# Kernel tuning notes

Hardware: AMD Instinct MI355X
Metric: run time of the kernel (lower is better)

The kernel has to match this reference:

```python
import jax, jax.numpy as jnp
import numpy as np

B, D, DEPTH, H, E, N, NC = 128, 192, 12, 3, 4, 65, 100
WIN_HALF = 3  # window_size=7 -> |i-j| <= 3


def _ln(x, g, b, eps=1e-5):
    m = x.mean(-1, keepdims=True)
    v = ((x - m) ** 2).mean(-1, keepdims=True)
    return (x - m) / jnp.sqrt(v + eps) * g + b


def _forward(x, conv_w, conv_b, pe_g, pe_b, cls_token, pos_embed,
             n1_g, n1_b, qkv_w, temp, proj_w, proj_b, n2_g, n2_b,
             gate_w, gate_b, e_w1, e_b1, e_w2, e_b2, attn_scale, mlp_scale,
             norm_g, norm_b, hc_w, hc_b, head_w, head_b):
    Bx = x.shape[0]
    # patch embed: conv with kernel==stride==4 is a blocked matmul
    p = x.reshape(Bx, 3, 8, 4, 8, 4).transpose(0, 2, 4, 1, 3, 5).reshape(Bx, 64, 48)
    t = p @ conv_w.reshape(D, 48).T + conv_b
    t = _ln(t, pe_g, pe_b)
    t = jnp.concatenate([jnp.broadcast_to(cls_token, (Bx, 1, D)), t], axis=1) + pos_embed
    Nn = t.shape[1]
    hd = D // H
    scale = hd ** -0.5
    idx = jnp.arange(Nn)
    # local-window attention mask (log of {0,1} -> {-inf,0})
    mask = jnp.where(jnp.abs(idx[:, None] - idx[None, :]) <= WIN_HALF, 0.0, -jnp.inf)
    for l in range(DEPTH):
        # --- attention ---
        y = _ln(t, n1_g[l], n1_b[l])
        qkv = (y @ qkv_w[l].T).reshape(Bx, Nn, 3, H, hd).transpose(2, 0, 3, 1, 4)
        q, k, v = qkv[0], qkv[1], qkv[2]
        a = (q @ k.transpose(0, 1, 3, 2)) * scale / temp[l]  # [B,H,N,N]
        a = jax.nn.softmax(a + mask, axis=-1)
        o = (a @ v).transpose(0, 2, 1, 3).reshape(Bx, Nn, D)
        o = o @ proj_w[l].T + proj_b[l]
        t = t + attn_scale[l] * o
        # --- top-2 MoE (dense-equivalent of the masked per-expert dispatch) ---
        y = _ln(t, n2_g[l], n2_b[l])
        g = jax.nn.softmax(y @ gate_w[l].T + gate_b[l], axis=-1)  # [B,N,E]
        tg, ti = jax.lax.top_k(g, 2)
        tg = tg / tg.sum(-1, keepdims=True)
        h = jax.nn.gelu(jnp.einsum('bnc,ehc->bneh', y, e_w1[l]) + e_b1[l], approximate=False)
        eo = jnp.einsum('bneh,ech->bnec', h, e_w2[l]) + e_b2[l]  # [B,N,E,C]
        sel = jnp.take_along_axis(eo, ti[..., None], axis=2)  # [B,N,2,C]
        mo = (sel * tg[..., None]).sum(axis=2)
        t = t + mlp_scale[l] * mo
    t = _ln(t, norm_g, norm_b)
    cls = t[:, 0]
    # hypercomplex linear head: out[:,k] += x[:,j] @ W[(k-j)%n].T
    xv = cls.reshape(Bx, E, D // E)
    perm = (jnp.arange(E)[:, None] - jnp.arange(E)[None, :]) % E  # [k,j] -> i
    hh = jnp.einsum('bjc,kjoc->bko', xv, hc_w[perm]).reshape(Bx, 2 * D) + hc_b
    hh = jax.nn.gelu(hh, approximate=False)
    return hh @ head_w.T + head_b


def setup_inputs() -> dict:
    ks = iter(jax.random.split(jax.random.key(0), 64))
    def rn(shape, s=0.02):
        return jax.random.normal(next(ks), shape, jnp.float32) * s
    return dict(
        x=jax.random.normal(next(ks), (B, 3, 32, 32), jnp.float32),
        conv_w=rn((D, 3, 4, 4)), conv_b=jnp.zeros((D,)),
        pe_g=jnp.ones((D,)), pe_b=jnp.zeros((D,)),
        cls_token=rn((1, 1, D)), pos_embed=rn((1, N, D)),
        n1_g=jnp.ones((DEPTH, D)), n1_b=jnp.zeros((DEPTH, D)),
        qkv_w=rn((DEPTH, 3 * D, D)), temp=jnp.ones((DEPTH, H, 1, 1)),
        proj_w=rn((DEPTH, D, D)), proj_b=jnp.zeros((DEPTH, D)),
        n2_g=jnp.ones((DEPTH, D)), n2_b=jnp.zeros((DEPTH, D)),
        gate_w=rn((DEPTH, E, D)), gate_b=jnp.zeros((DEPTH, E)),
        e_w1=rn((DEPTH, E, 2 * D, D)), e_b1=jnp.zeros((DEPTH, E, 2 * D)),
        e_w2=rn((DEPTH, E, D, 2 * D)), e_b2=jnp.zeros((DEPTH, E, D)),
        attn_scale=jnp.ones((DEPTH,)), mlp_scale=jnp.ones((DEPTH,)),
        norm_g=jnp.ones((D,)), norm_b=jnp.zeros((D,)),
        hc_w=rn((E, 2 * D // E, D // E)), hc_b=jnp.zeros((2 * D,)),
        head_w=rn((NC, 2 * D)), head_b=jnp.zeros((NC,)),
    )


def reference(x, conv_w, conv_b, pe_g, pe_b, cls_token, pos_embed,
              n1_g, n1_b, qkv_w, temp, proj_w, proj_b, n2_g, n2_b,
              gate_w, gate_b, e_w1, e_b1, e_w2, e_b2, attn_scale, mlp_scale,
              norm_g, norm_b, hc_w, hc_b, head_w, head_b):
    return _forward(x, conv_w, conv_b, pe_g, pe_b, cls_token, pos_embed,
                    n1_g, n1_b, qkv_w, temp, proj_w, proj_b, n2_g, n2_b,
                    gate_w, gate_b, e_w1, e_b1, e_w2, e_b2, attn_scale, mlp_scale,
                    norm_g, norm_b, hc_w, hc_b, head_w, head_b)
```

## Files before the change

### kernel.cpp

```cpp
#include <hip/hip_runtime.h>
#include <cmath>

#define ROWS 8320
#define DD   192

typedef __attribute__((ext_vector_type(8))) _Float16 half8;
typedef __attribute__((ext_vector_type(4))) float floatx4;

#define GLD16(gp, lp) __builtin_amdgcn_global_load_lds( \
    (const __attribute__((address_space(1))) void*)(gp), \
    (__attribute__((address_space(3))) void*)(lp), 16, 0, 0)

#define MFMA_F16 __builtin_amdgcn_mfma_f32_16x16x32_f16

__device__ __forceinline__ float gelu_f(float x) {
    return 0.5f * x * (1.0f + erff(x * 0.70710678118654752440f));
}

__device__ __forceinline__ float blk_sum_192(float v, float* sbuf) {
    int tid = threadIdx.x;
    sbuf[tid] = v;
    __syncthreads();
    for (int off = 96; off >= 3; off >>= 1) {
        if (tid < off) sbuf[tid] += sbuf[tid + off];
        __syncthreads();
    }
    float r = sbuf[0] + sbuf[1] + sbuf[2];
    __syncthreads();
    return r;
}

__global__ __launch_bounds__(256) void cvt_h_kernel(
    const float* __restrict__ s, _Float16* __restrict__ d, long n8)
{
    long i = (long)blockIdx.x * 256 + threadIdx.x;
    if (i >= n8) return;
    const float* sp = s + i * 8;
    _Float16* dp = d + i * 8;
    #pragma unroll
    for (int j = 0; j < 8; j++) dp[j] = (_Float16)sp[j];
}

__global__ __launch_bounds__(256) void permw2h_kernel(
    const float* __restrict__ s, _Float16* __restrict__ d)
{
    long i = (long)blockIdx.x * 256 + threadIdx.x;
    if (i >= (long)12 * 192 * 192) return;
    int l = (int)(i / (192 * 192));
    int rem = (int)(i % (192 * 192));
    int n = rem / 192, p = rem % 192;
    int c0 = p * 8;
    int e = c0 / 384, k0 = c0 % 384;
    const float* sp = s + (((size_t)l * 4 + e) * 192 + n) * 384 + k0;
    _Float16* dp = d + i * 8;
    #pragma unroll
    for (int j = 0; j < 8; j++) dp[j] = (_Float16)sp[j];
}

__global__ __launch_bounds__(192) void embed_kernel(
    const float* __restrict__ x, const float* __restrict__ conv_w,
    const float* __restrict__ conv_b, const float* __restrict__ pe_g,
    const float* __restrict__ pe_b, const float* __restrict__ cls_tok,
    const float* __restrict__ pos, float* __restrict__ t)
{
    __shared__ float patch[48];
    __shared__ float red[192];
    int blk = blockIdx.x;
    int b = blk / 65, n = blk % 65;
    int tid = threadIdx.x;
    if (n == 0) {
        t[(size_t)b * 65 * DD + tid] = cls_tok[tid] + pos[tid];
        return;
    }
    int p = n - 1, gy = p / 8, gx = p % 8;
    if (tid < 48) {
        int c = tid / 16, iy = (tid % 16) / 4, ix = tid % 4;
        patch[tid] = x[((size_t)b * 3 + c) * 1024 + (size_t)(gy * 4 + iy) * 32 + (gx * 4 + ix)];
    }
    __syncthreads();
    float s = conv_b[tid];
    const float* w = conv_w + (size_t)tid * 48;
    #pragma unroll
    for (int f = 0; f < 48; f++) s += patch[f] * w[f];
    float mean = blk_sum_192(s, red) * (1.0f / 192.0f);
    float d = s - mean;
    float var = blk_sum_192(d * d, red) * (1.0f / 192.0f);
    float o = d * rsqrtf(var + 1e-5f) * pe_g[tid] + pe_b[tid];
    t[((size_t)b * 65 + n) * DD + tid] = o + pos[(size_t)n * DD + tid];
}

__global__ __launch_bounds__(256) void ln_kernel(
    const float* __restrict__ in, const float* __restrict__ ctb,
    float* __restrict__ tout,
    float* __restrict__ yf, _Float16* __restrict__ yh,
    const float* __restrict__ g, const float* __restrict__ bb, long in_stride, int nrows,
    const float* __restrict__ gwm, const float* __restrict__ gb,
    int4* __restrict__ gwout)
{
    int wave = threadIdx.x >> 6, lane = threadIdx.x & 63;
    int r = blockIdx.x * 4 + wave;
    if (r >= nrows) return;
    const float* row = in + (size_t)r * in_stride;
    float v0 = row[lane], v1 = row[lane + 64], v2 = row[lane + 128];
    if (ctb) {
        long gr = (long)r * (in_stride / DD);
        const float* cb = ctb + gr * 384;
        v0 += cb[lane] + cb[192 + lane];
        v1 += cb[lane + 64] + cb[256 + lane];
        v2 += cb[lane + 128] + cb[320 + lane];
        if (tout) {
            float* tr = tout + (size_t)r * in_stride;
            tr[lane] = v0; tr[lane + 64] = v1; tr[lane + 128] = v2;
        }
    }
    float s = v0 + v1 + v2;
    #pragma unroll
    for (int off = 32; off > 0; off >>= 1) s += __shfl_xor(s, off);
    float mean = s * (1.0f / 192.0f);
    float d0 = v0 - mean, d1 = v1 - mean, d2 = v2 - mean;
    float q = d0 * d0 + d1 * d1 + d2 * d2;
    #pragma unroll
    for (int off = 32; off > 0; off >>= 1) q += __shfl_xor(q, off);
    float rstd = rsqrtf(q * (1.0f / 192.0f) + 1e-5f);
    float o0 = d0 * rstd * g[lane] + bb[lane];
    float o1 = d1 * rstd * g[lane + 64] + bb[lane + 64];
    float o2 = d2 * rstd * g[lane + 128] + bb[lane + 128];
    if (yf) {
        float* yr = yf + (size_t)r * DD;
        yr[lane] = o0; yr[lane + 64] = o1; yr[lane + 128] = o2;
    }
    if (yh) {
        _Float16* yr = yh + (size_t)r * DD;
        yr[lane] = (_Float16)o0; yr[lane + 64] = (_Float16)o1; yr[lane + 128] = (_Float16)o2;
    }
    if (gwm) {
        float pe[4];
        #pragma unroll
        for (int e = 0; e < 4; e++) {
            const float* w = gwm + (size_t)e * DD;
            pe[e] = o0 * w[lane] + o1 * w[lane + 64] + o2 * w[lane + 128];
            #pragma unroll
            for (int off = 32; off > 0; off >>= 1) pe[e] += __shfl_xor(pe[e], off);
        }
        if (lane == 0) {
            #pragma unroll
            for (int e = 0; e < 4; e++) pe[e] += gb[e];
            float mx = fmaxf(fmaxf(pe[0], pe[1]), fmaxf(pe[2], pe[3]));
            float ex[4];
            #pragma unroll
            for (int e = 0; e < 4; e++) ex[e] = expf(pe[e] - mx);
            int i0 = 0;
            #pragma unroll
            for (int e = 1; e < 4; e++) if (ex[e] > ex[i0]) i0 = e;
            int i1 = (i0 == 0) ? 1 : 0;
            #pragma unroll
            for (int e = 0; e < 4; e++) if (e != i0 && ex[e] > ex[i1]) i1 = e;
            float denom = ex[i0] + ex[i1];
            int4 o4;
            o4.x = i0; o4.y = i1;
            o4.z = __float_as_int(ex[i0] / denom);
            o4.w = __float_as_int(ex[i1] / denom);
            gwout[r] = o4;
        }
    }
}

__global__ __launch_bounds__(256) void gate_build_kernel(
    const int4* __restrict__ gwrow, int* __restrict__ cnt,
    int* __restrict__ list, float* __restrict__ wlist, int rows)
{
    int r = blockIdx.x * 256 + threadIdx.x;
    int lane = threadIdx.x & 63;
    bool active = r < rows;
    int4 gv = active ? gwrow[r] : int4{-1, -1, 0, 0};
    #pragma unroll
    for (int e = 0; e < 4; e++) {
        bool sel = active && (gv.x == e || gv.y == e);
        int rank = (gv.x == e) ? 0 : 1;
        float w = (gv.x == e) ? __int_as_float(gv.z) : __int_as_float(gv.w);
        unsigned long long mask = __ballot(sel);
        int cw = __popcll(mask);
        if (cw) {
            int leader = __ffsll((long long)mask) - 1;
            int base = 0;
            if (lane == leader) base = atomicAdd(&cnt[e], cw);
            base = __shfl(base, leader);
            if (sel) {
                int idx = base + __popcll(mask & ((1ULL << lane) - 1ULL));
                list[(size_t)e * ROWS + idx] = (r << 1) | rank;
                wlist[(size_t)e * ROWS + idx] = w;
            }
        }
    }
}

template <int MODE>
__global__ __launch_bounds__(256) void gemm_h(
    const _Float16* __restrict__ A, const _Float16* __restrict__ W,
    int Nn, _Float16* __restrict__ outH, float* __restrict__ t,
    const float* __restrict__ bias, const float* __restrict__ scale)
{
    __shared__ __align__(16) _Float16 As[64 * 192];
    __shared__ __align__(16) _Float16 Ws[64 * 192];
    const int tid = threadIdx.x;
    const int lane = tid & 63, wave = tid >> 6;
    const int m0 = blockIdx.x * 64, n0 = blockIdx.y * 64;
    const int wm = (wave & 1) * 32, wn = (wave >> 1) * 32;
    const int lr = lane & 15, quad = lane >> 4;

    #pragma unroll
    for (int i = 0; i < 6; i++) {
        int s = (wave * 6 + i) * 64 + lane;
        int rr = s / 24, c = s % 24;
        GLD16(A + (size_t)(m0 + rr) * 192 + (c ^ (rr & 7)) * 8,
              (char*)As + (size_t)(wave * 6 + i) * 1024);
        GLD16(W + (size_t)(n0 + rr) * 192 + (c ^ (rr & 7)) * 8,
              (char*)Ws + (size_t)(wave * 6 + i) * 1024);
    }
    __syncthreads();

    floatx4 zero = {0.f, 0.f, 0.f, 0.f};
    floatx4 acc[2][2];
    acc[0][0] = zero; acc[0][1] = zero; acc[1][0] = zero; acc[1][1] = zero;

    #pragma unroll
    for (int m = 0; m < 6; m++) {
        int ch = m * 4 + quad;
        half8 a[2], w[2];
        #pragma unroll
        for (int ti = 0; ti < 2; ti++) {
            int ar = wm + ti * 16 + lr;
            a[ti] = *(const half8*)(As + ((size_t)ar * 24 + (ch ^ (ar & 7))) * 8);
            int cr = wn + ti * 16 + lr;
            w[ti] = *(const half8*)(Ws + ((size_t)cr * 24 + (ch ^ (cr & 7))) * 8);
        }
        #pragma unroll
        for (int ti = 0; ti < 2; ti++)
            #pragma unroll
            for (int tj = 0; tj < 2; tj++)
                acc[ti][tj] = MFMA_F16(a[ti], w[tj], acc[ti][tj], 0, 0, 0);
    }

    float sc = (MODE == 2) ? scale[0] : 0.f;
    #pragma unroll
    for (int ti = 0; ti < 2; ti++)
        #pragma unroll
        for (int tj = 0; tj < 2; tj++)
            #pragma unroll
            for (int r = 0; r < 4; r++) {
                int grow = m0 + wm + ti * 16 + quad * 4 + r;
                int gcol = n0 + wn + tj * 16 + lr;
                float v = acc[ti][tj][r];
                if (MODE == 0) {
                    float vp = __shfl_xor(v, 1);
                    if ((lane & 1) == 0) {
                        union { _Float16 h[2]; unsigned u; } pk;
                        pk.h[0] = (_Float16)v;
                        pk.h[1] = (_Float16)vp;
                        *(unsigned*)(outH + (size_t)grow * Nn + (gcol & ~1)) = pk.u;
                    }
                } else {
                    t[(size_t)grow * DD + gcol] += sc * (v + bias[gcol]);
                }
            }
}

__global__ __launch_bounds__(256) void moe_kernel(
    const _Float16* __restrict__ yh, const _Float16* __restrict__ w1,
    const _Float16* __restrict__ w2, const float* __restrict__ b1,
    const float* __restrict__ b2, const float* __restrict__ scale,
    const int* __restrict__ cnt, const int* __restrict__ list,
    const float* __restrict__ wlist, float* __restrict__ ctb)
{
    __shared__ __align__(16) _Float16 As[32 * 192];
    __shared__ __align__(16) _Float16 W1s[64 * 192];
    __shared__ __align__(16) _Float16 W2s[192 * 64];
    __shared__ __align__(16) _Float16 Hs[32 * 64];
    __shared__ int   rl[32];
    __shared__ int   rk[32];
    __shared__ float wl[32];
    const int e  = blockIdx.y;
    const int cnte = cnt[e];
    const int r0 = blockIdx.x * 32;
    if (r0 >= cnte) return;
    const int tid = threadIdx.x;
    const int lane = tid & 63, wave = tid >> 6;
    const int lr = lane & 15, quad = lane >> 4;
    const int wr = (wave & 1) * 16;
    const int wc1 = (wave >> 1) * 16;
    const int wc2 = (wave >> 1) * 96;

    if (tid < 32) {
        int sl = r0 + tid;
        bool ok = sl < cnte;
        int v = ok ? list[(size_t)e * ROWS + sl] : 0;
        rl[tid] = ok ? (v >> 1) : 0;
        rk[tid] = ok ? (v & 1) : -1;
        wl[tid] = ok ? wlist[(size_t)e * ROWS + sl] : 0.f;
    }
    __syncthreads();

    #pragma unroll
    for (int i = 0; i < 3; i++) {
        int s = (wave * 3 + i) * 64 + lane;
        int rr = s / 24, c = s % 24;
        GLD16(yh + (size_t)rl[rr] * 192 + (c ^ (rr & 7)) * 8,
              (char*)As + (size_t)(wave * 3 + i) * 1024);
    }
    #pragma unroll
    for (int i = 0; i < 6; i++) {
        int s = (wave * 6 + i) * 64 + lane;
        int rr = s / 24, c = s % 24;
        GLD16(w1 + ((size_t)e * 384 + rr) * 192 + (c ^ (rr & 7)) * 8,
              (char*)W1s + (size_t)(wave * 6 + i) * 1024);
    }
    __syncthreads();

    floatx4 zero = {0.f, 0.f, 0.f, 0.f};
    floatx4 acc2[6];
    #pragma unroll
    for (int j = 0; j < 6; j++) acc2[j] = zero;

    for (int nc = 0; nc < 6; nc++) {
        int ncg = e * 6 + nc;
        #pragma unroll
        for (int i = 0; i < 6; i++) {
            int s = (wave * 6 + i) * 64 + lane;
            int n = s >> 3, c = s & 7;
            GLD16(w2 + (size_t)n * 1536 + (ncg * 8 + (c ^ (n & 7))) * 8,
                  (char*)W2s + (size_t)(wave * 6 + i) * 1024);
        }
        floatx4 acc1[2];
        acc1[0] = zero; acc1[1] = zero;
        #pragma unroll
        for (int m = 0; m < 6; m++) {
            int ar = wr + lr;
            int ch = m * 4 + quad;
            half8 a = *(const half8*)(As + ((size_t)ar * 24 + (ch ^ (ar & 7))) * 8);
            #pragma unroll
            for (int tc = 0; tc < 2; tc++) {
                int cr = wc1 + tc * 32 + lr;
                half8 w = *(const half8*)(W1s + ((size_t)cr * 24 + (ch ^ (cr & 7))) * 8);
                acc1[tc] = MFMA_F16(a, w, acc1[tc], 0, 0, 0);
            }
        }
        #pragma unroll
        for (int tc = 0; tc < 2; tc++)
            #pragma unroll
            for (int r = 0; r < 4; r++) {
                int hrow = wr + quad * 4 + r;
                int hcol = wc1 + tc * 32 + lr;
                float v = gelu_f(acc1[tc][r] + b1[64 * ncg + hcol]) * wl[hrow];
                float vp = __shfl_xor(v, 1);
                if ((lane & 1) == 0) {
                    union { _Float16 h[2]; unsigned u; } pk;
                    pk.h[0] = (_Float16)v;
                    pk.h[1] = (_Float16)vp;
                    int cl = (hcol >> 3) ^ (hrow & 7);
                    *(unsigned*)(Hs + ((size_t)hrow * 8 + cl) * 8 + (hcol & 7)) = pk.u;
                }
            }
        __syncthreads();
        if (nc < 5) {
            #pragma unroll
            for (int i = 0; i < 6; i++) {
                int s = (wave * 6 + i) * 64 + lane;
                int rr = s / 24, c = s % 24;
                GLD16(w1 + ((size_t)e * 384 + (nc + 1) * 64 + rr) * 192 + (c ^ (rr & 7)) * 8,
                      (char*)W1s + (size_t)(wave * 6 + i) * 1024);
            }
        }
        #pragma unroll
        for (int kk = 0; kk < 2; kk++) {
            int ar = wr + lr;
            int ch = kk * 4 + quad;
            half8 a = *(const half8*)(Hs + ((size_t)ar * 8 + (ch ^ (ar & 7))) * 8);
            #pragma unroll
            for (int tj = 0; tj < 6; tj++) {
                int cr = wc2 + tj * 16 + lr;
                half8 w = *(const half8*)(W2s + ((size_t)cr * 8 + (ch ^ (cr & 7))) * 8);
                acc2[tj] = MFMA_F16(a, w, acc2[tj], 0, 0, 0);
            }
        }
        __syncthreads();
    }

    float sc = scale[0];
    #pragma unroll
    for (int tj = 0; tj < 6; tj++) {
        int gcol = wc2 + tj * 16 + lr;
        #pragma unroll
        for (int r = 0; r < 4; r++) {
            int lrow = wr + quad * 4 + r;
            int rank = rk[lrow];
            if (rank >= 0) {
                float v = sc * (acc2[tj][r] + wl[lrow] * b2[e * 192 + gcol]);
                ctb[((size_t)rl[lrow] * 2 + rank) * 192 + gcol] = v;
            }
        }
    }
}

__global__ __launch_bounds__(256) void attn_kernel(
    const _Float16* __restrict__ qkv, const float* __restrict__ temp,
    _Float16* __restrict__ o)
{
    __shared__ float q[65][64], k[65][64], v[65][64];
    __shared__ float p[65][8];
    int bh = blockIdx.x;
    int b = bh / 3, h = bh % 3;
    int tid = threadIdx.x;
    float coef = 0.125f / temp[h];
    const _Float16* base = qkv + (size_t)b * 65 * 576 + h * 64;
    for (int idx = tid; idx < 65 * 64; idx += 256) {
        int i = idx >> 6, d = idx & 63;
        q[i][d] = (float)base[(size_t)i * 576 + d];
        k[i][d] = (float)base[(size_t)i * 576 + 192 + d];
        v[i][d] = (float)base[(size_t)i * 576 + 384 + d];
    }
    __syncthreads();
    if (tid < 65) {
        int i = tid;
        float sc[7];
        float mx = -1e30f;
        #pragma unroll
        for (int jo = 0; jo < 7; jo++) {
            int j = i - 3 + jo;
            if (j >= 0 && j < 65) {
                float s = 0.f;
                #pragma unroll
                for (int d = 0; d < 64; d++) s += q[i][d] * k[j][d];
                sc[jo] = s * coef;
                mx = fmaxf(mx, sc[jo]);
            } else sc[jo] = -1e30f;
        }
        float sum = 0.f;
        #pragma unroll
        for (int jo = 0; jo < 7; jo++) {
            float e = expf(sc[jo] - mx);
            p[i][jo] = e;
            sum += e;
        }
        float inv = 1.0f / sum;
        #pragma unroll
        for (int jo = 0; jo < 7; jo++) p[i][jo] *= inv;
    }
    __syncthreads();
    for (int idx = tid; idx < 65 * 64; idx += 256) {
        int i = idx >> 6, d = idx & 63;
        float s = 0.f;
        #pragma unroll
        for (int jo = 0; jo < 7; jo++) {
            int j = i - 3 + jo;
            if (j >= 0 && j < 65) s += p[i][jo] * v[j][d];
        }
        o[((size_t)b * 65 + i) * 192 + h * 64 + d] = (_Float16)s;
    }
}

__global__ __launch_bounds__(128) void head_kernel(
    const float* __restrict__ cls, const float* __restrict__ hc_w,
    const float* __restrict__ hc_b, const float* __restrict__ head_w,
    const float* __restrict__ head_b, float* __restrict__ out)
{
    __shared__ float c[192];
    __shared__ float hh[384];
    int b = blockIdx.x, tid = threadIdx.x;
    for (int i = tid; i < 192; i += 128) c[i] = cls[(size_t)b * 192 + i];
    __syncthreads();
    for (int i = tid; i < 384; i += 128) {
        int k = i / 96, o = i % 96;
        float s = hc_b[i];
        #pragma unroll
        for (int j = 0; j < 4; j++) {
            int pp = (k - j + 4) & 3;
            const float* w = hc_w + ((size_t)pp * 96 + o) * 48;
            const float* xv = c + j * 48;
            #pragma unroll
            for (int cc = 0; cc < 48; cc++) s += xv[cc] * w[cc];
        }
        hh[i] = gelu_f(s);
    }
    __syncthreads();
    for (int i = tid; i < 100; i += 128) {
        float s = head_b[i];
        const float* w = head_w + (size_t)i * 384;
        for (int kk = 0; kk < 384; kk++) s += hh[kk] * w[kk];
        out[(size_t)b * 100 + i] = s;
    }
}

extern "C" void kernel_launch(void* const* d_in, const int* in_sizes, int n_in,
                              void* d_out, int out_size, void* d_ws, size_t ws_size,
                              hipStream_t stream)
{
    const float* x        = (const float*)d_in[0];
    const float* conv_w   = (const float*)d_in[1];
    const float* conv_b   = (const float*)d_in[2];
    const float* pe_g     = (const float*)d_in[3];
    const float* pe_b     = (const float*)d_in[4];
    const float* cls_tok  = (const float*)d_in[5];
    const float* pos      = (const float*)d_in[6];
    const float* n1_g     = (const float*)d_in[7];
    const float* n1_b     = (const float*)d_in[8];
    const float* qkv_w    = (const float*)d_in[9];
    const float* temp     = (const float*)d_in[10];
    const float* proj_w   = (const float*)d_in[11];
    const float* proj_b   = (const float*)d_in[12];
    const float* n2_g     = (const float*)d_in[13];
    const float* n2_b     = (const float*)d_in[14];
    const float* gate_w   = (const float*)d_in[15];
    const float* gate_b   = (const float*)d_in[16];
    const float* e_w1     = (const float*)d_in[17];
    const float* e_b1     = (const float*)d_in[18];
    const float* e_w2     = (const float*)d_in[19];
    const float* e_b2     = (const float*)d_in[20];
    const float* attn_sc  = (const float*)d_in[21];
    const float* mlp_sc   = (const float*)d_in[22];
    const float* norm_g   = (const float*)d_in[23];
    const float* norm_b   = (const float*)d_in[24];
    const float* hc_w     = (const float*)d_in[25];
    const float* hc_b     = (const float*)d_in[26];
    const float* head_w   = (const float*)d_in[27];
    const float* head_b   = (const float*)d_in[28];

    char* base = (char*)d_ws;
    float*  t     = (float*)base;   base += (size_t)ROWS * DD * 4;
    float*  ctb   = (float*)base;   base += (size_t)ROWS * 384 * 4;
    int4*   gwrow = (int4*)base;    base += (size_t)ROWS * 16;
    int*    cnts  = (int*)base;     base += (size_t)12 * 4 * sizeof(int) + 64;
    int*    elist = (int*)base;     base += (size_t)4 * ROWS * 4;
    float*  ewls  = (float*)base;   base += (size_t)4 * ROWS * 4;
    float*  ycls  = (float*)base;   base += (size_t)128 * DD * 4;
    _Float16* yhb = (_Float16*)base; base += (size_t)ROWS * DD * 2;
    _Float16* qkvh = (_Float16*)base; base += (size_t)ROWS * 576 * 2;
    _Float16* osph = (_Float16*)base; base += (size_t)ROWS * DD * 2;
    _Float16* qkvw_h = (_Float16*)base; base += (size_t)12 * 576 * 192 * 2;
    _Float16* projw_h = (_Float16*)base; base += (size_t)12 * 192 * 192 * 2;
    _Float16* ew1_h = (_Float16*)base; base += (size_t)12 * 1536 * 192 * 2;
    _Float16* ew2_h = (_Float16*)base; base += (size_t)12 * 192 * 1536 * 2;

    hipMemsetAsync(cnts, 0, 12 * 4 * sizeof(int), stream);

    {
        long n8 = (long)12 * 576 * 192 / 8;
        cvt_h_kernel<<<(int)((n8 + 255) / 256), 256, 0, stream>>>(qkv_w, qkvw_h, n8);
        n8 = (long)12 * 192 * 192 / 8;
        cvt_h_kernel<<<(int)((n8 + 255) / 256), 256, 0, stream>>>(proj_w, projw_h, n8);
        n8 = (long)12 * 1536 * 192 / 8;
        cvt_h_kernel<<<(int)((n8 + 255) / 256), 256, 0, stream>>>(e_w1, ew1_h, n8);
        long n = (long)12 * 192 * 192;
        permw2h_kernel<<<(int)((n + 255) / 256), 256, 0, stream>>>(e_w2, ew2_h);
    }

    embed_kernel<<<128 * 65, 192, 0, stream>>>(x, conv_w, conv_b, pe_g, pe_b, cls_tok, pos, t);

    for (int l = 0; l < 12; l++) {
        ln_kernel<<<ROWS / 4, 256, 0, stream>>>(
            t, (l > 0) ? ctb : nullptr, (l > 0) ? t : nullptr,
            nullptr, yhb, n1_g + l * DD, n1_b + l * DD, DD, ROWS,
            nullptr, nullptr, nullptr);
        gemm_h<0><<<dim3(130, 9), 256, 0, stream>>>(
            yhb, qkvw_h + (size_t)l * 576 * 192, 576, qkvh, nullptr, nullptr, nullptr);
        attn_kernel<<<128 * 3, 256, 0, stream>>>(qkvh, temp + l * 3, osph);
        gemm_h<2><<<dim3(130, 3), 256, 0, stream>>>(
            osph, projw_h + (size_t)l * 192 * 192, 192, nullptr, t,
            proj_b + l * DD, attn_sc + l);
        ln_kernel<<<ROWS / 4, 256, 0, stream>>>(
            t, nullptr, nullptr, nullptr, yhb, n2_g + l * DD, n2_b + l * DD, DD, ROWS,
            gate_w + (size_t)l * 4 * DD, gate_b + l * 4, gwrow);
        gate_build_kernel<<<(ROWS + 255) / 256, 256, 0, stream>>>(
            gwrow, cnts + l * 4, elist, ewls, ROWS);
        moe_kernel<<<dim3(260, 4), 256, 0, stream>>>(
            yhb, ew1_h + (size_t)l * 1536 * 192, ew2_h + (size_t)l * 192 * 1536,
            e_b1 + (size_t)l * 1536, e_b2 + (size_t)l * 4 * 192, mlp_sc + l,
            cnts + l * 4, elist, ewls, ctb);
    }

    ln_kernel<<<32, 256, 0, stream>>>(
        t, ctb, nullptr, ycls, nullptr, norm_g, norm_b, (long)65 * DD, 128,
        nullptr, nullptr, nullptr);
    head_kernel<<<128, 128, 0, stream>>>(ycls, hc_w, hc_b, head_w, head_b, (float*)d_out);
}
```

Before: 1.352 ms.

## Scatter MoE output via atomics into residual and load A rows into registers

The MoE kernel now adds its expert outputs straight into the residual stream t with float atomicAdd. This replaces writing per-rank rows to a separate ctb buffer that the next layernorm had to read back and sum. It also loads each wave's gathered A rows straight from global memory into registers, dropping the LDS staging of activations and the shared row/weight tables. The attention kernel's shared arrays are padded to 65 columns to reduce bank conflicts. The cost is atomic contention on t, with two experts per row, and a summation order that is no longer deterministic.

Result: faster. 1.152 ms (-14.8%).

```diff
diff --git a/kernel.cpp b/kernel.cpp
--- a/kernel.cpp
+++ b/kernel.cpp
@@ -176,7 +176,6 @@
     #pragma unroll
     for (int e = 0; e < 4; e++) {
         bool sel = active && (gv.x == e || gv.y == e);
-        int rank = (gv.x == e) ? 0 : 1;
         float w = (gv.x == e) ? __int_as_float(gv.z) : __int_as_float(gv.w);
         unsigned long long mask = __ballot(sel);
         int cw = __popcll(mask);
@@ -187,6 +186,7 @@
             base = __shfl(base, leader);
             if (sel) {
                 int idx = base + __popcll(mask & ((1ULL << lane) - 1ULL));
+                int rank = (gv.x == e) ? 0 : 1;
                 list[(size_t)e * ROWS + idx] = (r << 1) | rank;
                 wlist[(size_t)e * ROWS + idx] = w;
             }
@@ -270,15 +270,11 @@
     const _Float16* __restrict__ w2, const float* __restrict__ b1,
     const float* __restrict__ b2, const float* __restrict__ scale,
     const int* __restrict__ cnt, const int* __restrict__ list,
-    const float* __restrict__ wlist, float* __restrict__ ctb)
-{
-    __shared__ __align__(16) _Float16 As[32 * 192];
+    const float* __restrict__ wlist, float* __restrict__ t)
+{
     __shared__ __align__(16) _Float16 W1s[64 * 192];
     __shared__ __align__(16) _Float16 W2s[192 * 64];
     __shared__ __align__(16) _Float16 Hs[32 * 64];
-    __shared__ int   rl[32];
-    __shared__ int   rk[32];
-    __shared__ float wl[32];
     const int e  = blockIdx.y;
     const int cnte = cnt[e];
     const int r0 = blockIdx.x * 32;
@@ -290,23 +286,6 @@
     const int wc1 = (wave >> 1) * 16;
     const int wc2 = (wave >> 1) * 96;
 
-    if (tid < 32) {
-        int sl = r0 + tid;
-        bool ok = sl < cnte;
-        int v = ok ? list[(size_t)e * ROWS + sl] : 0;
-        rl[tid] = ok ? (v >> 1) : 0;
-        rk[tid] = ok ? (v & 1) : -1;
-        wl[tid] = ok ? wlist[(size_t)e * ROWS + sl] : 0.f;
-    }
-    __syncthreads();
-
-    #pragma unroll
-    for (int i = 0; i < 3; i++) {
-        int s = (wave * 3 + i) * 64 + lane;
-        int rr = s / 24, c = s % 24;
-        GLD16(yh + (size_t)rl[rr] * 192 + (c ^ (rr & 7)) * 8,
-              (char*)As + (size_t)(wave * 3 + i) * 1024);
-    }
     #pragma unroll
     for (int i = 0; i < 6; i++) {
         int s = (wave * 6 + i) * 64 + lane;
@@ -314,6 +293,29 @@
         GLD16(w1 + ((size_t)e * 384 + rr) * 192 + (c ^ (rr & 7)) * 8,
               (char*)W1s + (size_t)(wave * 6 + i) * 1024);
     }
+
+    int sl = r0 + wr + lr;
+    int rv = -1; float wv = 0.f;
+    if (sl < cnte) {
+        rv = list[(size_t)e * ROWS + sl];
+        wv = wlist[(size_t)e * ROWS + sl];
+    }
+    int arow = (rv >= 0) ? (rv >> 1) : 0;
+
+    half8 a[6];
+    {
+        const _Float16* ap = yh + (size_t)arow * 192 + quad * 8;
+        #pragma unroll
+        for (int m = 0; m < 6; m++) a[m] = *(const half8*)(ap + m * 32);
+    }
+
+    int rvr[4]; float bwr[4];
+    #pragma unroll
+    for (int r = 0; r < 4; r++) {
+        rvr[r] = __shfl(rv, quad * 4 + r);
+        bwr[r] = __shfl(wv, quad * 4 + r);
+    }
+
     __syncthreads();
 
     floatx4 zero = {0.f, 0.f, 0.f, 0.f};
@@ -334,14 +336,12 @@
         acc1[0] = zero; acc1[1] = zero;
         #pragma unroll
         for (int m = 0; m < 6; m++) {
-            int ar = wr + lr;
             int ch = m * 4 + quad;
-            half8 a = *(const half8*)(As + ((size_t)ar * 24 + (ch ^ (ar & 7))) * 8);
             #pragma unroll
             for (int tc = 0; tc < 2; tc++) {
                 int cr = wc1 + tc * 32 + lr;
                 half8 w = *(const half8*)(W1s + ((size_t)cr * 24 + (ch ^ (cr & 7))) * 8);
-                acc1[tc] = MFMA_F16(a, w, acc1[tc], 0, 0, 0);
+                acc1[tc] = MFMA_F16(a[m], w, acc1[tc], 0, 0, 0);
             }
         }
         #pragma unroll
@@ -350,7 +350,7 @@
             for (int r = 0; r < 4; r++) {
                 int hrow = wr + quad * 4 + r;
                 int hcol = wc1 + tc * 32 + lr;
-                float v = gelu_f(acc1[tc][r] + b1[64 * ncg + hcol]) * wl[hrow];
+                float v = gelu_f(acc1[tc][r] + b1[64 * ncg + hcol]) * bwr[r];
                 float vp = __shfl_xor(v, 1);
                 if ((lane & 1) == 0) {
                     union { _Float16 h[2]; unsigned u; } pk;
@@ -374,12 +374,12 @@
         for (int kk = 0; kk < 2; kk++) {
             int ar = wr + lr;
             int ch = kk * 4 + quad;
-            half8 a = *(const half8*)(Hs + ((size_t)ar * 8 + (ch ^ (ar & 7))) * 8);
+            half8 ha = *(const half8*)(Hs + ((size_t)ar * 8 + (ch ^ (ar & 7))) * 8);
             #pragma unroll
             for (int tj = 0; tj < 6; tj++) {
                 int cr = wc2 + tj * 16 + lr;
                 half8 w = *(const half8*)(W2s + ((size_t)cr * 8 + (ch ^ (cr & 7))) * 8);
-                acc2[tj] = MFMA_F16(a, w, acc2[tj], 0, 0, 0);
+                acc2[tj] = MFMA_F16(ha, w, acc2[tj], 0, 0, 0);
             }
         }
         __syncthreads();
@@ -389,13 +389,12 @@
     #pragma unroll
     for (int tj = 0; tj < 6; tj++) {
         int gcol = wc2 + tj * 16 + lr;
+        float b2v = b2[e * 192 + gcol];
         #pragma unroll
         for (int r = 0; r < 4; r++) {
-            int lrow = wr + quad * 4 + r;
-            int rank = rk[lrow];
-            if (rank >= 0) {
-                float v = sc * (acc2[tj][r] + wl[lrow] * b2[e * 192 + gcol]);
-                ctb[((size_t)rl[lrow] * 2 + rank) * 192 + gcol] = v;
+            if (rvr[r] >= 0) {
+                float v = sc * (acc2[tj][r] + bwr[r] * b2v);
+                atomicAdd(&t[(size_t)(rvr[r] >> 1) * DD + gcol], v);
             }
         }
     }
@@ -405,7 +404,7 @@
     const _Float16* __restrict__ qkv, const float* __restrict__ temp,
     _Float16* __restrict__ o)
 {
-    __shared__ float q[65][64], k[65][64], v[65][64];
+    __shared__ float q[65][65], k[65][65], v[65][65];
     __shared__ float p[65][8];
     int bh = blockIdx.x;
     int b = bh / 3, h = bh % 3;
@@ -469,11 +468,11 @@
     for (int i = tid; i < 192; i += 128) c[i] = cls[(size_t)b * 192 + i];
     __syncthreads();
     for (int i = tid; i < 384; i += 128) {
-        int k = i / 96, o = i % 96;
+        int kx = i / 96, o = i % 96;
         float s = hc_b[i];
         #pragma unroll
         for (int j = 0; j < 4; j++) {
-            int pp = (k - j + 4) & 3;
+            int pp = (kx - j + 4) & 3;
             const float* w = hc_w + ((size_t)pp * 96 + o) * 48;
             const float* xv = c + j * 48;
             #pragma unroll
@@ -526,7 +525,6 @@
 
     char* base = (char*)d_ws;
     float*  t     = (float*)base;   base += (size_t)ROWS * DD * 4;
-    float*  ctb   = (float*)base;   base += (size_t)ROWS * 384 * 4;
     int4*   gwrow = (int4*)base;    base += (size_t)ROWS * 16;
     int*    cnts  = (int*)base;     base += (size_t)12 * 4 * sizeof(int) + 64;
     int*    elist = (int*)base;     base += (size_t)4 * ROWS * 4;
@@ -557,7 +555,7 @@
 
     for (int l = 0; l < 12; l++) {
         ln_kernel<<<ROWS / 4, 256, 0, stream>>>(
-            t, (l > 0) ? ctb : nullptr, (l > 0) ? t : nullptr,
+            t, nullptr, nullptr,
             nullptr, yhb, n1_g + l * DD, n1_b + l * DD, DD, ROWS,
             nullptr, nullptr, nullptr);
         gemm_h<0><<<dim3(130, 9), 256, 0, stream>>>(
@@ -574,11 +572,11 @@
         moe_kernel<<<dim3(260, 4), 256, 0, stream>>>(
             yhb, ew1_h + (size_t)l * 1536 * 192, ew2_h + (size_t)l * 192 * 1536,
             e_b1 + (size_t)l * 1536, e_b2 + (size_t)l * 4 * 192, mlp_sc + l,
-            cnts + l * 4, elist, ewls, ctb);
+            cnts + l * 4, elist, ewls, t);
     }
 
     ln_kernel<<<32, 256, 0, stream>>>(
-        t, ctb, nullptr, ycls, nullptr, norm_g, norm_b, (long)65 * DD, 128,
+        t, nullptr, nullptr, ycls, nullptr, norm_g, norm_b, (long)65 * DD, 128,
         nullptr, nullptr, nullptr);
     head_kernel<<<128, 128, 0, stream>>>(ycls, hc_w, hc_b, head_w, head_b, (float*)d_out);
 }
```
